# Performance work log

Hardware: AMD Instinct MI355X
Metric: run time of the kernel (lower is better)

The kernel has to match this reference:

```python
import jax, jax.numpy as jnp
import numpy as np

EPS = 1e-6
BLK = 16  # NVFP4 block size (16 elements share one e4m3 scale)
# e2m1 representable magnitudes and rounding midpoints
GRID = jnp.array([0.0, 0.5, 1.0, 1.5, 2.0, 3.0, 4.0, 6.0], dtype=jnp.float32)
MID = jnp.array([0.25, 0.75, 1.25, 1.75, 2.5, 3.5, 5.0], dtype=jnp.float32)


def _e2m1(x):
    # round magnitude to nearest e2m1 grid point (saturate at 6.0)
    a = jnp.minimum(jnp.abs(x), 6.0)
    idx = jnp.searchsorted(MID, a, side='right')
    return jnp.sign(x) * jnp.take(GRID, idx)


def _fp4_quant_scaled(x, gscale):
    # vllm scaled_fp4_quant: per-16 block amax -> e4m3 block scale (scaled by
    # global scale), quantize to e2m1. Returns q * s8 (= dequant * gscale).
    m, n = x.shape
    xb = x.reshape(m, n // BLK, BLK)
    amax = jnp.max(jnp.abs(xb), axis=-1, keepdims=True)
    s8 = (amax * gscale / 6.0).astype(jnp.float8_e4m3fn).astype(jnp.float32)
    safe = jnp.where(s8 > 0, s8, 1.0)
    q = _e2m1(jnp.where(s8 > 0, xb * gscale / safe, 0.0))
    return (q * s8).reshape(m, n)


def _fp4_mm(y, w, ag, wg):
    # cutlass_scaled_fp4_mm with alpha = 1/(ag*wg): dequantized matmul y @ w.T
    alpha = 1.0 / (ag * wg)
    yq = _fp4_quant_scaled(y, ag)   # [m, h]
    wq = _fp4_quant_scaled(w, wg)   # [h, h]
    return (yq @ wq.T) * alpha


def _rmsnorm(x, w):
    v = jnp.mean(x * x, axis=-1, keepdims=True)
    return x * jax.lax.rsqrt(v + EPS) * w


def setup_inputs() -> dict:
    key = jax.random.key(0)
    k1, k2, k3, k4 = jax.random.split(key, 4)
    T, H = 8192, 4096
    hidden_states = jax.random.normal(k1, (T, H), dtype=jnp.float32)
    norm_w = jnp.ones((4, H), dtype=jnp.float32)          # RMSNorm weights (init ones)
    w = jax.random.uniform(k2, (3, H, H), dtype=jnp.float32)     # torch.rand
    agscale = jax.random.uniform(k3, (3,), dtype=jnp.float32, minval=0.25, maxval=1.0)
    wgscale = jax.random.uniform(k4, (3,), dtype=jnp.float32, minval=0.25, maxval=1.0)
    return {"hidden_states": hidden_states, "norm_w": norm_w, "w": w,
            "agscale": agscale, "wgscale": wgscale}


def reference(hidden_states, norm_w, w, agscale, wgscale):
    # tensor_model_parallel_all_reduce == identity on a single device
    x = jnp.maximum(hidden_states, 0.0)  # relu
    resid = x
    y = _rmsnorm(x, norm_w[0])
    for i in range(3):  # 3 structurally distinct layers (fixed small loop)
        z = _fp4_mm(y, w[i], agscale[i], wgscale[i])
        resid = z + resid                # fused add
        y = _rmsnorm(resid, norm_w[i + 1])
    return y
```

## Files before the change

kernel.cpp:

```cpp
#include <hip/hip_runtime.h>
#include <stdint.h>

#define HD 4096
#define TD 8192

typedef unsigned short u16;
typedef unsigned int u32;
typedef __bf16 bf16x8 __attribute__((ext_vector_type(8)));
typedef float f32x4 __attribute__((ext_vector_type(4)));

#define GL16(gp, lp) __builtin_amdgcn_global_load_lds( \
    (__attribute__((address_space(1))) void*)(void*)(uintptr_t)(gp), \
    (__attribute__((address_space(3))) void*)(lp), 16, 0, 0)


__device__ __forceinline__ float e4m3_rtne(float f) {
  if (f <= 0.0f) return 0.0f;
  unsigned u = __float_as_uint(f);
  int e = (int)((u >> 23) & 0xff) - 127;
  if (e < -6) e = -6;
  float C = __uint_as_float((unsigned)(e + 147) << 23);
  float r = (f + C) - C;
  return fminf(r, 448.0f);
}

__device__ __forceinline__ void quant_store16(const float v[16], float g, u16* dst) {
  float amax = 0.0f;
#pragma unroll
  for (int j = 0; j < 16; ++j) amax = fmaxf(amax, fabsf(v[j]));
  float s = e4m3_rtne(amax * g / 6.0f);
  u32 out[8];
  if (s > 0.0f) {
    const float m1 = 0.25f * s, m2 = 0.75f * s, m3 = 1.25f * s, m4 = 1.75f * s;
    const float m5 = 2.5f * s, m6 = 3.5f * s, m7 = 5.0f * s;
#pragma unroll
    for (int p = 0; p < 8; ++p) {
      u16 b[2];
#pragma unroll
      for (int h = 0; h < 2; ++h) {
        float t = v[2 * p + h] * g;
        float u = fabsf(t);
        float q = (u < m4) ? ((u < m2) ? ((u < m1) ? 0.0f : 0.5f)
                                       : ((u < m3) ? 1.0f : 1.5f))
                           : ((u < m6) ? ((u < m5) ? 2.0f : 3.0f)
                                       : ((u < m7) ? 4.0f : 6.0f));
        float val = copysignf(q * s, t);
        b[h] = (u16)(__float_as_uint(val) >> 16);
      }
      out[p] = (u32)b[0] | ((u32)b[1] << 16);
    }
  } else {
#pragma unroll
    for (int p = 0; p < 8; ++p) out[p] = 0u;
  }
  uint4* d4 = (uint4*)dst;
  d4[0] = make_uint4(out[0], out[1], out[2], out[3]);
  d4[1] = make_uint4(out[4], out[5], out[6], out[7]);
}


__global__ __launch_bounds__(256) void k_relu_norm_quant(
    const float* __restrict__ hs, const float* __restrict__ nw,
    const float* __restrict__ agp, float* __restrict__ resid,
    u16* __restrict__ yq) {
  const int lane = threadIdx.x & 63;
  const int row = blockIdx.x * 4 + (threadIdx.x >> 6);
  const size_t base = (size_t)row * HD;
  float v[64];
#pragma unroll
  for (int c = 0; c < 4; ++c)
#pragma unroll
    for (int j = 0; j < 4; ++j)
      ((float4*)v)[c * 4 + j] =
          ((const float4*)(hs + base + c * 1024 + lane * 16))[j];
  float ss = 0.0f;
#pragma unroll
  for (int j = 0; j < 64; ++j) {
    v[j] = fmaxf(v[j], 0.0f);
    ss += v[j] * v[j];
  }
#pragma unroll
  for (int c = 0; c < 4; ++c)
#pragma unroll
    for (int j = 0; j < 4; ++j)
      ((float4*)(resid + base + c * 1024 + lane * 16))[j] = ((float4*)v)[c * 4 + j];
#pragma unroll
  for (int off = 32; off > 0; off >>= 1) ss += __shfl_xor(ss, off, 64);
  const float rs = 1.0f / sqrtf(ss * (1.0f / HD) + 1e-6f);
  const float g = agp[0];
  const float* nwp = nw;
#pragma unroll
  for (int c = 0; c < 4; ++c) {
    float y[16];
#pragma unroll
    for (int j = 0; j < 16; ++j)
      y[j] = v[c * 16 + j] * rs * nwp[c * 1024 + lane * 16 + j];
    quant_store16(y, g, yq + base + c * 1024 + lane * 16);
  }
}

__global__ __launch_bounds__(256) void k_norm_quant(
    const float* __restrict__ resid, const float* __restrict__ nw,
    const float* __restrict__ agp, int li, u16* __restrict__ yq) {
  const int lane = threadIdx.x & 63;
  const int row = blockIdx.x * 4 + (threadIdx.x >> 6);
  const size_t base = (size_t)row * HD;
  float v[64];
#pragma unroll
  for (int c = 0; c < 4; ++c)
#pragma unroll
    for (int j = 0; j < 4; ++j)
      ((float4*)v)[c * 4 + j] =
          ((const float4*)(resid + base + c * 1024 + lane * 16))[j];
  float ss = 0.0f;
#pragma unroll
  for (int j = 0; j < 64; ++j) ss += v[j] * v[j];
#pragma unroll
  for (int off = 32; off > 0; off >>= 1) ss += __shfl_xor(ss, off, 64);
  const float rs = 1.0f / sqrtf(ss * (1.0f / HD) + 1e-6f);
  const float g = agp[li];
  const float* nwp = nw + (size_t)li * HD;
#pragma unroll
  for (int c = 0; c < 4; ++c) {
    float y[16];
#pragma unroll
    for (int j = 0; j < 16; ++j)
      y[j] = v[c * 16 + j] * rs * nwp[c * 1024 + lane * 16 + j];
    quant_store16(y, g, yq + base + c * 1024 + lane * 16);
  }
}

__global__ __launch_bounds__(256) void k_final_norm(
    float* __restrict__ io, const float* __restrict__ nw) {
  const int lane = threadIdx.x & 63;
  const int row = blockIdx.x * 4 + (threadIdx.x >> 6);
  const size_t base = (size_t)row * HD;
  float v[64];
#pragma unroll
  for (int c = 0; c < 4; ++c)
#pragma unroll
    for (int j = 0; j < 4; ++j)
      ((float4*)v)[c * 4 + j] =
          ((const float4*)(io + base + c * 1024 + lane * 16))[j];
  float ss = 0.0f;
#pragma unroll
  for (int j = 0; j < 64; ++j) ss += v[j] * v[j];
#pragma unroll
  for (int off = 32; off > 0; off >>= 1) ss += __shfl_xor(ss, off, 64);
  const float rs = 1.0f / sqrtf(ss * (1.0f / HD) + 1e-6f);
  const float* nwp = nw + (size_t)3 * HD;
#pragma unroll
  for (int c = 0; c < 4; ++c) {
#pragma unroll
    for (int j = 0; j < 16; ++j)
      v[c * 16 + j] = v[c * 16 + j] * rs * nwp[c * 1024 + lane * 16 + j];
#pragma unroll
    for (int j = 0; j < 4; ++j)
      ((float4*)(io + base + c * 1024 + lane * 16))[j] = ((float4*)v)[c * 4 + j];
  }
}

__global__ __launch_bounds__(256) void k_quant_w(
    const float* __restrict__ w, const float* __restrict__ wgp, int li,
    u16* __restrict__ wq) {
  const int row = blockIdx.x, tid = threadIdx.x;
  const size_t base = (size_t)li * HD * HD + (size_t)row * HD + tid * 16;
  float v[16];
#pragma unroll
  for (int j = 0; j < 4; ++j) ((float4*)v)[j] = ((const float4*)(w + base))[j];
  quant_store16(v, wgp[li], wq + (size_t)row * HD + tid * 16);
}

__global__ __launch_bounds__(256) void k_quant_w_all(
    const float* __restrict__ w, const float* __restrict__ wgp,
    u16* __restrict__ wq3) {
  const int row = blockIdx.x, tid = threadIdx.x;
  const size_t base = (size_t)row * HD + tid * 16;
  float v[16];
#pragma unroll
  for (int j = 0; j < 4; ++j) ((float4*)v)[j] = ((const float4*)(w + base))[j];
  quant_store16(v, wgp[row >> 12], wq3 + base);
}


#define BARF() do { asm volatile("" ::: "memory"); \
    __builtin_amdgcn_s_barrier(); \
    asm volatile("" ::: "memory"); } while (0)
#define WLG() asm volatile("s_waitcnt lgkmcnt(0)" ::: "memory")
#define WVM6() asm volatile("s_waitcnt vmcnt(6)" ::: "memory")

__global__ __launch_bounds__(512, 2) void k_gemm(
    const u16* __restrict__ A, const u16* __restrict__ B,
    float* __restrict__ resid, const float* __restrict__ agp,
    const float* __restrict__ wgp, int layer) {
  __shared__ __align__(16) u16 ldsA[2 * 256 * 64];
  __shared__ __align__(16) u16 ldsB[2 * 256 * 64];
  const int tid = threadIdx.x;
  const int lane = tid & 63, wave = tid >> 6;
  const int wr = wave >> 2, wc = wave & 3;
  const int r = lane & 15, q = lane >> 4;

  int bid = blockIdx.x;
  bid = (bid & 7) * 64 + (bid >> 3);
  const int m0 = (bid >> 4) * 256;
  const int n0 = (bid & 15) * 256;

  const int rs = tid >> 3;
  const int cs = ((tid & 7) ^ (rs & 7)) * 8;
  const u16* gA = A + (size_t)(m0 + rs) * HD + cs;
  const u16* gB = B + (size_t)(n0 + rs) * HD + cs;
  u16* lA = ldsA + tid * 8;
  u16* lB = ldsB + tid * 8;

#define STG_A(bb, h, koff) do { \
    GL16(gA + (size_t)(h) * (128 * HD) + (koff), lA + (bb) + (h) * 8192); \
    GL16(gA + (size_t)(h) * (128 * HD) + 64 * HD + (koff), lA + (bb) + (h) * 8192 + 4096); \
  } while (0)
#define STG_B(bb, h, koff) do { \
    GL16(gB + (size_t)(h) * (128 * HD) + (koff), lB + (bb) + (h) * 8192); \
    GL16(gB + (size_t)(h) * (128 * HD) + 64 * HD + (koff), lB + (bb) + (h) * 8192 + 4096); \
  } while (0)

  const int sa = (q ^ (r & 7)) * 8;
  const int sb = ((q + 4) ^ (r & 7)) * 8;
  const int arow = (wr * 128 + r) * 64;
  const int brow = (wc * 64 + r) * 64;

  f32x4 acc[8][4];
#pragma unroll
  for (int i = 0; i < 8; ++i)
#pragma unroll
    for (int j = 0; j < 4; ++j) acc[i][j] = (f32x4){0.f, 0.f, 0.f, 0.f};

  bf16x8 a[4][2], b[4][2];

#define LD_A(base) do { \
    _Pragma("unroll") \
    for (int mi = 0; mi < 4; ++mi) { \
      a[mi][0] = *(const bf16x8*)((base) + arow + mi * 1024 + sa); \
      a[mi][1] = *(const bf16x8*)((base) + arow + mi * 1024 + sb); \
    } } while (0)
#define LD_B(base) do { \
    _Pragma("unroll") \
    for (int nj = 0; nj < 4; ++nj) { \
      b[nj][0] = *(const bf16x8*)((base) + brow + nj * 1024 + sa); \
      b[nj][1] = *(const bf16x8*)((base) + brow + nj * 1024 + sb); \
    } } while (0)
#define MMQ(mh, nh) do { \
    _Pragma("unroll") \
    for (int mi = 0; mi < 4; ++mi) \
    _Pragma("unroll") \
    for (int nj = 0; nj < 2; ++nj) { \
      acc[(mh) * 4 + mi][(nh) * 2 + nj] = __builtin_amdgcn_mfma_f32_16x16x32_bf16( \
          a[mi][0], b[(nh) * 2 + nj][0], acc[(mh) * 4 + mi][(nh) * 2 + nj], 0, 0, 0); \
      acc[(mh) * 4 + mi][(nh) * 2 + nj] = __builtin_amdgcn_mfma_f32_16x16x32_bf16( \
          a[mi][1], b[(nh) * 2 + nj][1], acc[(mh) * 4 + mi][(nh) * 2 + nj], 0, 0, 0); \
    } } while (0)

  STG_B(0, 0, 0); STG_B(0, 1, 0);
  STG_A(0, 0, 0); STG_A(0, 1, 0);
  STG_B(16384, 0, 64); STG_B(16384, 1, 64);
  STG_A(16384, 0, 64);
  WVM6();
  BARF();

  for (int i = 0; i < 32; ++i) {
    const int kb = i * 128;
    const int k1 = kb + 64;
    int k2 = kb + 128; if (k2 >= HD) k2 -= HD;
    int k3 = kb + 192; if (k3 >= HD) k3 -= HD;
    LD_A(ldsA); LD_B(ldsB);
    STG_A(16384, 1, k1);
    BARF(); WLG();
    __builtin_amdgcn_s_setprio(1); MMQ(0, 0); __builtin_amdgcn_s_setprio(0);
    BARF();
    STG_B(0, 0, k2);
    BARF();
    __builtin_amdgcn_s_setprio(1); MMQ(0, 1); __builtin_amdgcn_s_setprio(0);
    BARF();
    LD_A(ldsA + 4096);
    STG_B(0, 1, k2);
    BARF(); WLG();
    __builtin_amdgcn_s_setprio(1); MMQ(1, 0); __builtin_amdgcn_s_setprio(0);
    BARF();
    STG_A(0, 0, k2);
    WVM6();
    BARF();
    __builtin_amdgcn_s_setprio(1); MMQ(1, 1); __builtin_amdgcn_s_setprio(0);
    BARF();
    LD_A(ldsA + 16384); LD_B(ldsB + 16384);
    STG_A(0, 1, k2);
    BARF(); WLG();
    __builtin_amdgcn_s_setprio(1); MMQ(0, 0); __builtin_amdgcn_s_setprio(0);
    BARF();
    STG_B(16384, 0, k3);
    BARF();
    __builtin_amdgcn_s_setprio(1); MMQ(0, 1); __builtin_amdgcn_s_setprio(0);
    BARF();
    LD_A(ldsA + 16384 + 4096);
    STG_B(16384, 1, k3);
    BARF(); WLG();
    __builtin_amdgcn_s_setprio(1); MMQ(1, 0); __builtin_amdgcn_s_setprio(0);
    BARF();
    STG_A(16384, 0, k3);
    WVM6();
    BARF();
    __builtin_amdgcn_s_setprio(1); MMQ(1, 1); __builtin_amdgcn_s_setprio(0);
    BARF();
  }

  const float alpha = 1.0f / (agp[layer] * wgp[layer]);
#pragma unroll
  for (int mi = 0; mi < 8; ++mi) {
    const int gm0 = m0 + wr * 128 + mi * 16 + q * 4;
#pragma unroll
    for (int nj = 0; nj < 4; ++nj) {
      const int gn = n0 + wc * 64 + nj * 16 + r;
#pragma unroll
      for (int t = 0; t < 4; ++t) {
        float* p = resid + (size_t)(gm0 + t) * HD + gn;
        *p = fmaf(acc[mi][nj][t], alpha, *p);
      }
    }
  }
}


extern "C" void kernel_launch(void* const* d_in, const int* in_sizes, int n_in,
                              void* d_out, int out_size, void* d_ws, size_t ws_size,
                              hipStream_t stream) {
  const float* hs = (const float*)d_in[0];
  const float* nw = (const float*)d_in[1];
  const float* w = (const float*)d_in[2];
  const float* ag = (const float*)d_in[3];
  const float* wg = (const float*)d_in[4];
  float* out = (float*)d_out;

  const size_t need_big = ((size_t)3 * HD * HD + (size_t)TD * HD) * sizeof(u16);
  if (ws_size >= need_big) {
    u16* wq3 = (u16*)d_ws;
    u16* yq = wq3 + (size_t)3 * HD * HD;
    k_quant_w_all<<<3 * HD, 256, 0, stream>>>(w, wg, wq3);
    k_relu_norm_quant<<<TD / 4, 256, 0, stream>>>(hs, nw, ag, out, yq);
    for (int l = 0; l < 3; ++l) {
      k_gemm<<<dim3((TD / 256) * (HD / 256)), 512, 0, stream>>>(
          yq, wq3 + (size_t)l * HD * HD, out, ag, wg, l);
      if (l < 2) k_norm_quant<<<TD / 4, 256, 0, stream>>>(out, nw, ag, l + 1, yq);
    }
  } else {
    u16* wq = (u16*)d_ws;
    u16* yq = (u16*)d_ws + (size_t)HD * HD;
    k_relu_norm_quant<<<TD / 4, 256, 0, stream>>>(hs, nw, ag, out, yq);
    for (int l = 0; l < 3; ++l) {
      k_quant_w<<<HD, 256, 0, stream>>>(w, wg, l, wq);
      k_gemm<<<dim3((TD / 256) * (HD / 256)), 512, 0, stream>>>(yq, wq, out, ag, wg, l);
      if (l < 2) k_norm_quant<<<TD / 4, 256, 0, stream>>>(out, nw, ag, l + 1, yq);
    }
  }
  k_final_norm<<<TD / 4, 256, 0, stream>>>(out, nw);
}
```

Baseline: 1.356 ms.

## Restructure GEMM main loop into four coarser phases with fewer barriers

```diff
diff --git a/kernel.cpp b/kernel.cpp
--- a/kernel.cpp
+++ b/kernel.cpp
@@ -187,7 +187,7 @@
     __builtin_amdgcn_s_barrier(); \
     asm volatile("" ::: "memory"); } while (0)
 #define WLG() asm volatile("s_waitcnt lgkmcnt(0)" ::: "memory")
-#define WVM6() asm volatile("s_waitcnt vmcnt(6)" ::: "memory")
+#define WVM4() asm volatile("s_waitcnt vmcnt(4)" ::: "memory")
 
 __global__ __launch_bounds__(512, 2) void k_gemm(
     const u16* __restrict__ A, const u16* __restrict__ B,
@@ -234,11 +234,11 @@
 
   bf16x8 a[4][2], b[4][2];
 
-#define LD_A(base) do { \
+#define LD_AH(base, mh) do { \
     _Pragma("unroll") \
     for (int mi = 0; mi < 4; ++mi) { \
-      a[mi][0] = *(const bf16x8*)((base) + arow + mi * 1024 + sa); \
-      a[mi][1] = *(const bf16x8*)((base) + arow + mi * 1024 + sb); \
+      a[mi][0] = *(const bf16x8*)((base) + arow + (mh) * 4096 + mi * 1024 + sa); \
+      a[mi][1] = *(const bf16x8*)((base) + arow + (mh) * 4096 + mi * 1024 + sb); \
     } } while (0)
 #define LD_B(base) do { \
     _Pragma("unroll") \
@@ -260,8 +260,7 @@
   STG_B(0, 0, 0); STG_B(0, 1, 0);
   STG_A(0, 0, 0); STG_A(0, 1, 0);
   STG_B(16384, 0, 64); STG_B(16384, 1, 64);
-  STG_A(16384, 0, 64);
-  WVM6();
+  WVM4();
   BARF();
 
   for (int i = 0; i < 32; ++i) {
@@ -269,43 +268,31 @@
     const int k1 = kb + 64;
     int k2 = kb + 128; if (k2 >= HD) k2 -= HD;
     int k3 = kb + 192; if (k3 >= HD) k3 -= HD;
-    LD_A(ldsA); LD_B(ldsB);
-    STG_A(16384, 1, k1);
-    BARF(); WLG();
-    __builtin_amdgcn_s_setprio(1); MMQ(0, 0); __builtin_amdgcn_s_setprio(0);
-    BARF();
-    STG_B(0, 0, k2);
-    BARF();
-    __builtin_amdgcn_s_setprio(1); MMQ(0, 1); __builtin_amdgcn_s_setprio(0);
-    BARF();
-    LD_A(ldsA + 4096);
-    STG_B(0, 1, k2);
-    BARF(); WLG();
-    __builtin_amdgcn_s_setprio(1); MMQ(1, 0); __builtin_amdgcn_s_setprio(0);
-    BARF();
-    STG_A(0, 0, k2);
-    WVM6();
-    BARF();
-    __builtin_amdgcn_s_setprio(1); MMQ(1, 1); __builtin_amdgcn_s_setprio(0);
-    BARF();
-    LD_A(ldsA + 16384); LD_B(ldsB + 16384);
-    STG_A(0, 1, k2);
-    BARF(); WLG();
-    __builtin_amdgcn_s_setprio(1); MMQ(0, 0); __builtin_amdgcn_s_setprio(0);
-    BARF();
-    STG_B(16384, 0, k3);
-    BARF();
-    __builtin_amdgcn_s_setprio(1); MMQ(0, 1); __builtin_amdgcn_s_setprio(0);
-    BARF();
-    LD_A(ldsA + 16384 + 4096);
-    STG_B(16384, 1, k3);
-    BARF(); WLG();
-    __builtin_amdgcn_s_setprio(1); MMQ(1, 0); __builtin_amdgcn_s_setprio(0);
-    BARF();
-    STG_A(16384, 0, k3);
-    WVM6();
-    BARF();
-    __builtin_amdgcn_s_setprio(1); MMQ(1, 1); __builtin_amdgcn_s_setprio(0);
+    LD_AH(ldsA, 0); LD_B(ldsB);
+    STG_A(16384, 0, k1); STG_A(16384, 1, k1);
+    BARF();
+    __builtin_amdgcn_s_setprio(1); MMQ(0, 0); MMQ(0, 1); __builtin_amdgcn_s_setprio(0);
+    WLG();
+    BARF();
+    LD_AH(ldsA, 1);
+    STG_B(0, 0, k2); STG_B(0, 1, k2);
+    WVM4();
+    BARF();
+    __builtin_amdgcn_s_setprio(1); MMQ(1, 0); MMQ(1, 1); __builtin_amdgcn_s_setprio(0);
+    WLG();
+    BARF();
+    LD_AH(ldsA + 16384, 0); LD_B(ldsB + 16384);
+    STG_A(0, 0, k2); STG_A(0, 1, k2);
+    BARF();
+    __builtin_amdgcn_s_setprio(1); MMQ(0, 0); MMQ(0, 1); __builtin_amdgcn_s_setprio(0);
+    WLG();
+    BARF();
+    LD_AH(ldsA + 16384, 1);
+    STG_B(16384, 0, k3); STG_B(16384, 1, k3);
+    WVM4();
+    BARF();
+    __builtin_amdgcn_s_setprio(1); MMQ(1, 0); MMQ(1, 1); __builtin_amdgcn_s_setprio(0);
+    WLG();
     BARF();
   }
 
```

After: 1.350 ms. About the same (-0.5%).
